# Kernel tuning notes

Measured on AMD Instinct MI355X. Metric: run time of the kernel, lower is better.

Reference implementation:

```python
import jax, jax.numpy as jnp
import numpy as np
import math

B, N, K, C_IN, C_OUT = 2, 16384, 16, 128, 128


def _gather_neighbors(x, idx):
    # x: [B, N, C], idx: [B, N, K] -> [B, N, K, C]
    return jax.vmap(lambda xb, ib: xb[ib])(x, idx)


def setup_inputs() -> dict:
    key = jax.random.key(0)
    k1, k2, k3 = jax.random.split(key, 3)
    x = jax.random.normal(k1, (B, N, C_IN), dtype=jnp.float32)
    edge_index = jax.random.randint(k2, (2, B, N, K), 0, N, dtype=jnp.int64)
    W = jax.random.normal(k3, (C_OUT, C_IN), dtype=jnp.float32) * (1.0 / math.sqrt(C_IN))
    b = jnp.zeros((C_OUT,), dtype=jnp.float32)
    return {"x": x, "edge_index": edge_index, "W": W, "b": b}


def reference(x, edge_index, W, b):
    # x: [B, N, C]; edge_index: [2, B, N, K]
    x_i = _gather_neighbors(x, edge_index[1])  # [B, N, K, C] (centers)
    x_j = _gather_neighbors(x, edge_index[0])  # [B, N, K, C] (neighbors)
    scale = 1.0 / math.sqrt(x_i.shape[-1])
    scores = jnp.einsum('bnkc,bnjc->bnkj', x_i, x_j) * scale  # [B, N, K, K]
    p_attn = jax.nn.softmax(scores, axis=-1)
    h_k = jnp.einsum('bnkj,bnjc->bnkc', p_attn, x_j).sum(axis=-2)  # [B, N, C]
    y = (x + h_k) @ W.T + b  # Linear(in_channels -> out_channels)
    return jax.nn.relu(y)
```

## Files before the change

### kernel.cpp

```cpp
#include <hip/hip_runtime.h>
#include <hip/hip_bf16.h>
#include <math.h>

#define BB 2
#define NN 16384
#define KK 16
#define CC 128
#define COUT 128
#define NODES (BB * NN)

typedef __attribute__((ext_vector_type(8))) short bf16x8;
typedef __attribute__((ext_vector_type(4))) float f32x4;

__device__ __forceinline__ bf16x8 cvt8(f32x4 a, f32x4 b) {
    union { bf16x8 v; __hip_bfloat162 h[4]; } u;
    u.h[0] = __float22bfloat162_rn(make_float2(a[0], a[1]));
    u.h[1] = __float22bfloat162_rn(make_float2(a[2], a[3]));
    u.h[2] = __float22bfloat162_rn(make_float2(b[0], b[1]));
    u.h[3] = __float22bfloat162_rn(make_float2(b[2], b[3]));
    return u.v;
}

template <int CTRL>
__device__ __forceinline__ float rot_add(float v) {
    int r = __builtin_amdgcn_update_dpp(0, __float_as_int(v), CTRL, 0xF, 0xF, true);
    return v + __int_as_float(r);
}
__device__ __forceinline__ float row16_sum(float v) {
    v = rot_add<0x128>(v); v = rot_add<0x124>(v);
    v = rot_add<0x122>(v); v = rot_add<0x121>(v);
    return v;
}
__device__ __forceinline__ float row16_sum4(float v) {
    v = rot_add<0x128>(v); v = rot_add<0x124>(v);
    return v;
}

__global__ __launch_bounds__(256) void cast_x(
    const float* __restrict__ x, __hip_bfloat16* __restrict__ xh)
{
    const int i = blockIdx.x * 256 + threadIdx.x;
    const f32x4* p = (const f32x4*)(x + (size_t)i * 8);
    f32x4 a = p[0], b = p[1];
    *(bf16x8*)(xh + (size_t)i * 8) = cvt8(a, b);
}

__global__ __launch_bounds__(256) void attn_phase(
    const float* __restrict__ x,
    const __hip_bfloat16* __restrict__ xh,
    const int* __restrict__ edge,
    __hip_bfloat16* __restrict__ z)
{
    __shared__ float hbuf[4][4 * 132];

    const int t = threadIdx.x;
    const int wv = t >> 6;
    const int lane = t & 63;
    const int m = lane & 15;
    const int q = lane >> 4;
    const int node = blockIdx.x * 4 + wv;
    const int b = node >> 14;
    const __hip_bfloat16* xbh = xh + (size_t)b * (NN * CC);

    const size_t ebase = (size_t)node * KK + m;
    const int idx_j = edge[ebase];
    const int idx_i = edge[(size_t)(NODES * KK) + ebase];

    const __hip_bfloat16* pi = xbh + (size_t)idx_i * CC + q * 8;
    const __hip_bfloat16* pj = xbh + (size_t)idx_j * CC + q * 8;
    bf16x8 afr[4], bfr[4];
    #pragma unroll
    for (int s = 0; s < 4; ++s) {
        afr[s] = *(const bf16x8*)(pi + 32 * s);
        bfr[s] = *(const bf16x8*)(pj + 32 * s);
    }

    f32x4 acc = {0.f, 0.f, 0.f, 0.f};
    #pragma unroll
    for (int s = 0; s < 4; ++s)
        acc = __builtin_amdgcn_mfma_f32_16x16x32_bf16(afr[s], bfr[s], acc, 0, 0, 0);

    const float scale = 0.08838834764831843f;
    float w_part = 0.f;
    #pragma unroll
    for (int i = 0; i < 4; ++i) {
        float e = __expf(acc[i] * scale);
        float s = row16_sum(e);
        w_part += e * (1.0f / s);
    }
    w_part += __shfl_xor(w_part, 16, 64);
    w_part += __shfl_xor(w_part, 32, 64);
    const float wj = w_part;

    #pragma unroll
    for (int s = 0; s < 4; ++s) {
        union { bf16x8 v; unsigned short u[8]; } ub;
        ub.v = bfr[s];
        float f[8];
        #pragma unroll
        for (int e = 0; e < 8; ++e) {
            f[e] = __uint_as_float((unsigned)ub.u[e] << 16) * wj;
            f[e] = row16_sum4(f[e]);
        }
        if (m < 4) {
            f32x4 lo = {f[0], f[1], f[2], f[3]};
            f32x4 hi = {f[4], f[5], f[6], f[7]};
            *(f32x4*)&hbuf[wv][m * 132 + 32 * s + 8 * q]     = lo;
            *(f32x4*)&hbuf[wv][m * 132 + 32 * s + 8 * q + 4] = hi;
        }
    }
    float hx = 0.f, hy = 0.f;
    #pragma unroll
    for (int r = 0; r < 4; ++r) {
        float2 v = *(const float2*)&hbuf[wv][r * 132 + 2 * lane];
        hx += v.x; hy += v.y;
    }

    const float* xb = x + (size_t)b * (NN * CC);
    const int n_self = node & (NN - 1);
    float2 xc = *(const float2*)(xb + (size_t)n_self * CC + 2 * lane);
    __hip_bfloat162 zz = __float22bfloat162_rn(make_float2(xc.x + hx, xc.y + hy));
    *(__hip_bfloat162*)(z + (size_t)node * CC + 2 * lane) = zz;
}

__global__ __launch_bounds__(256, 4) void linear_relu(
    const __hip_bfloat16* __restrict__ z,
    const float* __restrict__ W,
    const float* __restrict__ bias,
    float* __restrict__ out)
{
    const int t = threadIdx.x;
    const int lane = t & 63;
    const int wid = blockIdx.x * 4 + (t >> 6);
    const int ntile = wid & 7;
    const int m0 = wid >> 3;
    const int nm = lane & 15;
    const int nq = lane >> 4;

    const float* wp = W + (size_t)(ntile * 16 + nm) * CC + nq * 8;
    bf16x8 bfr[4];
    #pragma unroll
    for (int s = 0; s < 4; ++s) {
        f32x4 w0 = *(const f32x4*)(wp + 32 * s);
        f32x4 w1 = *(const f32x4*)(wp + 32 * s + 4);
        bfr[s] = cvt8(w0, w1);
    }
    const float bv = bias[ntile * 16 + nm];

    #pragma unroll
    for (int it = 0; it < 4; ++it) {
        const int mt = m0 + it * 512;
        const __hip_bfloat16* zp = z + (size_t)(mt * 16 + nm) * CC + nq * 8;
        bf16x8 afr[4];
        #pragma unroll
        for (int s = 0; s < 4; ++s)
            afr[s] = *(const bf16x8*)(zp + 32 * s);
        f32x4 acc = {0.f, 0.f, 0.f, 0.f};
        #pragma unroll
        for (int s = 0; s < 4; ++s)
            acc = __builtin_amdgcn_mfma_f32_16x16x32_bf16(afr[s], bfr[s], acc, 0, 0, 0);
        float* op = out + (size_t)(mt * 16 + nq * 4) * COUT + ntile * 16 + nm;
        #pragma unroll
        for (int i = 0; i < 4; ++i)
            op[(size_t)i * COUT] = fmaxf(acc[i] + bv, 0.f);
    }
}

extern "C" void kernel_launch(void* const* d_in, const int* in_sizes, int n_in,
                              void* d_out, int out_size, void* d_ws, size_t ws_size,
                              hipStream_t stream) {
    const float* x    = (const float*)d_in[0];
    const int*   edge = (const int*)d_in[1];
    const float* W    = (const float*)d_in[2];
    const float* bias = (const float*)d_in[3];
    float* out = (float*)d_out;
    __hip_bfloat16* z  = (__hip_bfloat16*)d_ws;
    __hip_bfloat16* xh = (__hip_bfloat16*)d_ws + (size_t)NODES * CC;

    cast_x<<<(NODES * CC) / (256 * 8), 256, 0, stream>>>(x, xh);
    attn_phase<<<NODES / 4, 256, 0, stream>>>(x, xh, edge, z);
    linear_relu<<<1024, 256, 0, stream>>>(z, W, bias, out);
}
```

Baseline: 124.7 us.

## Stage gathered rows through LDS with full-row coalesced loads, read self from bf16 copy

The attention kernel now gathers each neighbor row with 16 lanes reading a contiguous 256-byte bf16 row, instead of 4 lanes each taking scattered 16-byte chunks. The rows are staged in padded shared memory and the MFMA fragments are read back from there. The self term is read from the bf16 copy rather than the fp32 input, which cuts traffic but adds bf16 rounding to x. Edge-index and cast loads use nontemporal hints, and the softmax divide uses a fast reciprocal. The new shared-memory staging adds about 35KB of LDS per block, which may lower occupancy.

```diff
diff --git a/kernel.cpp b/kernel.cpp
--- a/kernel.cpp
+++ b/kernel.cpp
@@ -8,6 +8,7 @@
 #define CC 128
 #define COUT 128
 #define NODES (BB * NN)
+#define SP 136
 
 typedef __attribute__((ext_vector_type(8))) short bf16x8;
 typedef __attribute__((ext_vector_type(4))) float f32x4;
@@ -41,57 +42,27 @@
 {
     const int i = blockIdx.x * 256 + threadIdx.x;
     const f32x4* p = (const f32x4*)(x + (size_t)i * 8);
-    f32x4 a = p[0], b = p[1];
+    f32x4 a = __builtin_nontemporal_load(p);
+    f32x4 b = __builtin_nontemporal_load(p + 1);
     *(bf16x8*)(xh + (size_t)i * 8) = cvt8(a, b);
 }
 
-__global__ __launch_bounds__(256) void attn_phase(
-    const float* __restrict__ x,
-    const __hip_bfloat16* __restrict__ xh,
-    const int* __restrict__ edge,
-    __hip_bfloat16* __restrict__ z)
-{
-    __shared__ float hbuf[4][4 * 132];
-
-    const int t = threadIdx.x;
-    const int wv = t >> 6;
-    const int lane = t & 63;
-    const int m = lane & 15;
-    const int q = lane >> 4;
-    const int node = blockIdx.x * 4 + wv;
-    const int b = node >> 14;
-    const __hip_bfloat16* xbh = xh + (size_t)b * (NN * CC);
-
-    const size_t ebase = (size_t)node * KK + m;
-    const int idx_j = edge[ebase];
-    const int idx_i = edge[(size_t)(NODES * KK) + ebase];
-
-    const __hip_bfloat16* pi = xbh + (size_t)idx_i * CC + q * 8;
-    const __hip_bfloat16* pj = xbh + (size_t)idx_j * CC + q * 8;
-    bf16x8 afr[4], bfr[4];
-    #pragma unroll
-    for (int s = 0; s < 4; ++s) {
-        afr[s] = *(const bf16x8*)(pi + 32 * s);
-        bfr[s] = *(const bf16x8*)(pj + 32 * s);
-    }
-
-    f32x4 acc = {0.f, 0.f, 0.f, 0.f};
-    #pragma unroll
-    for (int s = 0; s < 4; ++s)
-        acc = __builtin_amdgcn_mfma_f32_16x16x32_bf16(afr[s], bfr[s], acc, 0, 0, 0);
-
+__device__ __forceinline__ float col_weight(f32x4 acc) {
     const float scale = 0.08838834764831843f;
-    float w_part = 0.f;
+    float w = 0.f;
     #pragma unroll
     for (int i = 0; i < 4; ++i) {
         float e = __expf(acc[i] * scale);
         float s = row16_sum(e);
-        w_part += e * (1.0f / s);
-    }
-    w_part += __shfl_xor(w_part, 16, 64);
-    w_part += __shfl_xor(w_part, 32, 64);
-    const float wj = w_part;
-
+        w += e * __builtin_amdgcn_rcpf(s);
+    }
+    w += __shfl_xor(w, 16, 64);
+    w += __shfl_xor(w, 32, 64);
+    return w;
+}
+
+__device__ __forceinline__ float2 reduce_h(const bf16x8* bfr, float wj,
+                                           float* hb, int m, int q, int lane) {
     #pragma unroll
     for (int s = 0; s < 4; ++s) {
         union { bf16x8 v; unsigned short u[8]; } ub;
@@ -105,22 +76,82 @@
         if (m < 4) {
             f32x4 lo = {f[0], f[1], f[2], f[3]};
             f32x4 hi = {f[4], f[5], f[6], f[7]};
-            *(f32x4*)&hbuf[wv][m * 132 + 32 * s + 8 * q]     = lo;
-            *(f32x4*)&hbuf[wv][m * 132 + 32 * s + 8 * q + 4] = hi;
+            *(f32x4*)&hb[m * 132 + 32 * s + 8 * q]     = lo;
+            *(f32x4*)&hb[m * 132 + 32 * s + 8 * q + 4] = hi;
         }
     }
     float hx = 0.f, hy = 0.f;
     #pragma unroll
     for (int r = 0; r < 4; ++r) {
-        float2 v = *(const float2*)&hbuf[wv][r * 132 + 2 * lane];
+        float2 v = *(const float2*)&hb[r * 132 + 2 * lane];
         hx += v.x; hy += v.y;
     }
-
-    const float* xb = x + (size_t)b * (NN * CC);
-    const int n_self = node & (NN - 1);
-    float2 xc = *(const float2*)(xb + (size_t)n_self * CC + 2 * lane);
-    __hip_bfloat162 zz = __float22bfloat162_rn(make_float2(xc.x + hx, xc.y + hy));
-    *(__hip_bfloat162*)(z + (size_t)node * CC + 2 * lane) = zz;
+    return make_float2(hx, hy);
+}
+
+__global__ __launch_bounds__(256) void attn_phase(
+    const __hip_bfloat16* __restrict__ xh,
+    const int* __restrict__ edge,
+    __hip_bfloat16* __restrict__ z)
+{
+    __shared__ __hip_bfloat16 stg[4][32 * SP];
+    __shared__ float hbuf[4][4 * 132];
+
+    const int t = threadIdx.x;
+    const int wv = t >> 6;
+    const int lane = t & 63;
+    const int m = lane & 15;
+    const int q = lane >> 4;
+    const int r = lane >> 4;
+    const int c = lane & 15;
+
+    const int node = blockIdx.x * 4 + wv;
+    const int b = node >> 14;
+    const __hip_bfloat16* xbh = xh + (size_t)b * (size_t)(NN * CC);
+    __hip_bfloat16* sw = &stg[wv][0];
+
+    const int* ej = edge + (size_t)node * KK;
+    const int* ei = ej + (size_t)NODES * KK;
+
+    bf16x8 ld[8];
+    #pragma unroll
+    for (int g = 0; g < 4; ++g) {
+        int ridx = __builtin_nontemporal_load(ei + g * 4 + r);
+        ld[g] = *(const bf16x8*)(xbh + (size_t)ridx * CC + c * 8);
+    }
+    #pragma unroll
+    for (int g = 0; g < 4; ++g) {
+        int ridx = __builtin_nontemporal_load(ej + g * 4 + r);
+        ld[4 + g] = *(const bf16x8*)(xbh + (size_t)ridx * CC + c * 8);
+    }
+    #pragma unroll
+    for (int g = 0; g < 4; ++g)
+        *(bf16x8*)(sw + (g * 4 + r) * SP + c * 8) = ld[g];
+    #pragma unroll
+    for (int g = 0; g < 4; ++g)
+        *(bf16x8*)(sw + (16 + g * 4 + r) * SP + c * 8) = ld[4 + g];
+
+    bf16x8 afr[4], bfr[4];
+    #pragma unroll
+    for (int s = 0; s < 4; ++s) {
+        afr[s] = *(const bf16x8*)(sw + m * SP + s * 32 + q * 8);
+        bfr[s] = *(const bf16x8*)(sw + (16 + m) * SP + s * 32 + q * 8);
+    }
+
+    f32x4 acc = {0.f, 0.f, 0.f, 0.f};
+    #pragma unroll
+    for (int s = 0; s < 4; ++s)
+        acc = __builtin_amdgcn_mfma_f32_16x16x32_bf16(afr[s], bfr[s], acc, 0, 0, 0);
+
+    const float wj = col_weight(acc);
+
+    float2 h = reduce_h(bfr, wj, &hbuf[wv][0], m, q, lane);
+
+    const int n0 = node & (NN - 1);
+    __hip_bfloat162 rx = *(const __hip_bfloat162*)(xbh + (size_t)n0 * CC + 2 * lane);
+    float2 xc = __bfloat1622float2(rx);
+    *(__hip_bfloat162*)(z + (size_t)node * CC + 2 * lane) =
+        __float22bfloat162_rn(make_float2(xc.x + h.x, xc.y + h.y));
 }
 
 __global__ __launch_bounds__(256, 4) void linear_relu(
@@ -178,6 +209,6 @@
     __hip_bfloat16* xh = (__hip_bfloat16*)d_ws + (size_t)NODES * CC;
 
     cast_x<<<(NODES * CC) / (256 * 8), 256, 0, stream>>>(x, xh);
-    attn_phase<<<NODES / 4, 256, 0, stream>>>(x, xh, edge, z);
+    attn_phase<<<NODES / 4, 256, 0, stream>>>(xh, edge, z);
     linear_relu<<<1024, 256, 0, stream>>>(z, W, bias, out);
 }
```

Measured after the change: 121.0 us. 3.0% less time.
